# Optimization experiments

Hardware: AMD Instinct MI355X
Metric: run time of the kernel (lower is better)

The kernel has to match this reference:

```python
import jax, jax.numpy as jnp
import numpy as np

B, S, D, H, E = 2, 1024, 1024, 4096, 8


def _xavier(key, shape):
    # matches torch.nn.init.xavier_uniform_ on a 3D tensor: fan_in/out from last two dims
    fan_in, fan_out = shape[-2], shape[-1]
    limit = float(np.sqrt(6.0 / (fan_in + fan_out)))
    return jax.random.uniform(key, shape, jnp.float32, -limit, limit)


def setup_inputs() -> dict:
    key = jax.random.key(0)
    ks = jax.random.split(key, 4)
    x = jax.random.normal(ks[0], (B, S, D), jnp.float32)
    router_w = jax.random.normal(ks[1], (D, E), jnp.float32) * (1.0 / np.sqrt(D))
    router_b = jnp.zeros((E,), jnp.float32)
    fc1_weight = _xavier(ks[2], (E, D, H))
    fc1_bias = jnp.zeros((E, H), jnp.float32)
    fc2_weight = _xavier(ks[3], (E, H, D))
    fc2_bias = jnp.zeros((E, D), jnp.float32)
    return {
        "x": x,
        "router_w": router_w,
        "router_b": router_b,
        "fc1_weight": fc1_weight,
        "fc1_bias": fc1_bias,
        "fc2_weight": fc2_weight,
        "fc2_bias": fc2_bias,
    }


def reference(x, router_w, router_b, fc1_weight, fc1_bias, fc2_weight, fc2_bias):
    b, s, d = x.shape
    x_flat = x.reshape(-1, d)                                  # [T, D]
    logits = x_flat @ router_w + router_b                       # [T, E]
    probs = jax.nn.softmax(logits, axis=-1)                     # [T, E]
    # per-expert FC1 + exact GELU (torch nn.GELU default is erf-based)
    h = jnp.einsum('td,edh->teh', x_flat, fc1_weight) + fc1_bias  # [T, E, H]
    h = jax.nn.gelu(h, approximate=False)
    expert_out = jnp.einsum('teh,ehd->ted', h, fc2_weight) + fc2_bias  # [T, E, D]
    out_flat = jnp.einsum('te,ted->td', probs, expert_out)      # [T, D]
    y = out_flat.reshape(b, s, d)
    router_probs = probs.reshape(b, s, -1)
    return y, router_probs
```

## Files before the change

kernel.cpp:

```cpp
#include <hip/hip_runtime.h>
#include <math.h>


typedef float f32x4 __attribute__((ext_vector_type(4)));
typedef __bf16 bf16x8 __attribute__((ext_vector_type(8)));

#define GLL16(gp, lp)                                                          \
  __builtin_amdgcn_global_load_lds(                                            \
      (const __attribute__((address_space(1))) void*)(gp),                     \
      (__attribute__((address_space(3))) void*)(lp), 16, 0, 0)

__device__ __forceinline__ float gelu_f(float h) {
  return 0.5f * h * (1.f + erff(h * 0.70710678118654752f));
}

__global__ void router_kernel(const float* __restrict__ x,
                              const float* __restrict__ rw,
                              const float* __restrict__ rb,
                              float* __restrict__ P,
                              float* __restrict__ probs_out)
{
  int gid = blockIdx.x * blockDim.x + threadIdx.x;
  int t = gid >> 6;
  int l = gid & 63;
  const float* xr = x + (size_t)t * 1024;
  float a[8];
#pragma unroll
  for (int e = 0; e < 8; ++e) a[e] = 0.f;
  for (int d = l; d < 1024; d += 64) {
    float xv = xr[d];
    f32x4 w0 = *(const f32x4*)(rw + d * 8);
    f32x4 w1 = *(const f32x4*)(rw + d * 8 + 4);
#pragma unroll
    for (int e = 0; e < 4; ++e) a[e] += xv * w0[e];
#pragma unroll
    for (int e = 0; e < 4; ++e) a[4 + e] += xv * w1[e];
  }
#pragma unroll
  for (int off = 32; off > 0; off >>= 1) {
#pragma unroll
    for (int e = 0; e < 8; ++e) a[e] += __shfl_down(a[e], off);
  }
  if (l == 0) {
#pragma unroll
    for (int e = 0; e < 8; ++e) a[e] += rb[e];
    float m = a[0];
#pragma unroll
    for (int e = 1; e < 8; ++e) m = fmaxf(m, a[e]);
    float s = 0.f;
#pragma unroll
    for (int e = 0; e < 8; ++e) { a[e] = __expf(a[e] - m); s += a[e]; }
    float inv = 1.f / s;
#pragma unroll
    for (int e = 0; e < 8; ++e) {
      float p = a[e] * inv;
      if (P) P[t * 8 + e] = p;
      probs_out[t * 8 + e] = p;
    }
  }
}

__global__ void cvt_kernel(const float* __restrict__ src,
                           __bf16* __restrict__ dst)
{
  size_t i = ((size_t)blockIdx.x * 256 + threadIdx.x) * 8;
  f32x4 v0 = *(const f32x4*)(src + i);
  f32x4 v1 = *(const f32x4*)(src + i + 4);
  bf16x8 o;
#pragma unroll
  for (int j = 0; j < 4; ++j) o[j] = (__bf16)v0[j];
#pragma unroll
  for (int j = 0; j < 4; ++j) o[4 + j] = (__bf16)v1[j];
  *(bf16x8*)(dst + i) = o;
}

__global__ void transconv_kernel(const float* __restrict__ src,
                                 __bf16* __restrict__ dst,
                                 int R, int C, int cChunk,
                                 size_t dstLd, size_t zOff)
{
  size_t bs = (size_t)blockIdx.z * (size_t)R * (size_t)C;
  size_t dzo = (size_t)blockIdx.z * zOff;
  int r = blockIdx.x * 256 + threadIdx.x;
  int c0 = blockIdx.y * cChunk;
  const float* s = src + bs + (size_t)r * C;
  for (int c = c0; c < c0 + cChunk; c += 8) {
    f32x4 v0 = *(const f32x4*)(s + c);
    f32x4 v1 = *(const f32x4*)(s + c + 4);
    float vv[8] = {v0[0], v0[1], v0[2], v0[3], v1[0], v1[1], v1[2], v1[3]};
#pragma unroll
    for (int j = 0; j < 8; ++j)
      dst[(size_t)(c + j) * dstLd + dzo + r] = (__bf16)vv[j];
  }
}

__device__ __forceinline__ void mfma_loop256(
    const char* Ab, const char* Bb, size_t ldaB, size_t ldbB, int K,
    char* lds, f32x4 acc[8][4])
{
  const int tid = threadIdx.x;
  const int w = tid >> 6, l = tid & 63;
  const int wm = w >> 2, wn = w & 3;
  const int m16 = l & 15, q = l >> 4;
  const int posB = ((q ^ ((m16 >> 1) & 3)) << 4);
  const int aE = (wm * 128 + m16) * 64 + posB;
  const int bE = 16384 + (wn * 64 + m16) * 64 + posB;
  const int sc16 = (((l & 3) ^ ((l >> 3) & 3)) << 4);
  const size_t sAoff = (size_t)(w * 32 + (l >> 2)) * ldaB + sc16;
  const size_t sBoff = (size_t)(w * 32 + (l >> 2)) * ldbB + sc16;
  const int ldst = w * 32 * 64;
  const int NT = K >> 5;

#define STAGE256(u)                                                            \
  {                                                                            \
    char* dA = lds + (((u) & 3) * 32768) + ldst;                               \
    const char* gA = Ab + sAoff + ((size_t)(u) << 6);                          \
    GLL16(gA, dA);                                                             \
    GLL16(gA + 16 * ldaB, dA + 1024);                                          \
    char* dB = dA + 16384;                                                     \
    const char* gB = Bb + sBoff + ((size_t)(u) << 6);                          \
    GLL16(gB, dB);                                                             \
    GLL16(gB + 16 * ldbB, dB + 1024);                                          \
  }

#define KFRAGS(T)                                                              \
    const char* ring = lds + (((T) & 3) * 32768);                              \
    bf16x8 af[8], bv[4];                                                       \
    _Pragma("unroll") for (int mi = 0; mi < 8; ++mi)                           \
        af[mi] = *(const bf16x8*)(ring + aE + mi * 1024);                      \
    _Pragma("unroll") for (int nj = 0; nj < 4; ++nj)                           \
        bv[nj] = *(const bf16x8*)(ring + bE + nj * 1024);

#define KMFMA                                                                  \
    __builtin_amdgcn_sched_barrier(0);                                         \
    asm volatile("s_waitcnt lgkmcnt(0)" ::: "memory");                         \
    __builtin_amdgcn_sched_barrier(0);                                         \
    __builtin_amdgcn_s_setprio(1);                                             \
    _Pragma("unroll") for (int mi = 0; mi < 8; ++mi)                           \
      _Pragma("unroll") for (int nj = 0; nj < 4; ++nj)                         \
        acc[mi][nj] = __builtin_amdgcn_mfma_f32_16x16x32_bf16(                 \
            af[mi], bv[nj], acc[mi][nj], 0, 0, 0);                             \
    __builtin_amdgcn_s_setprio(0);                                             \
    __builtin_amdgcn_sched_barrier(0);

  STAGE256(0);
  STAGE256(1);
  STAGE256(2);
  asm volatile("s_waitcnt vmcnt(8)" ::: "memory");
  __builtin_amdgcn_s_barrier();

  int t = 0;
  for (; t < NT - 3; ++t) {
    KFRAGS(t);
    STAGE256(t + 3);
    KMFMA;
    asm volatile("s_waitcnt vmcnt(8)" ::: "memory");
    __builtin_amdgcn_s_barrier();
  }
  {
    KFRAGS(t);
    KMFMA;
    asm volatile("s_waitcnt vmcnt(0)" ::: "memory");
    __builtin_amdgcn_s_barrier();
  }
  ++t;
  {
    KFRAGS(t);
    KMFMA;
  }
  ++t;
  {
    KFRAGS(t);
    KMFMA;
  }
#undef STAGE256
#undef KFRAGS
#undef KMFMA
}

__device__ __forceinline__ int xcd_swz(int id, int nwg) {
  return ((nwg & 7) == 0) ? ((id & 7) * (nwg >> 3) + (id >> 3)) : id;
}

__global__ __launch_bounds__(512, 2) void gemm1_kernel(
    const __bf16* __restrict__ X, const __bf16* __restrict__ W1T,
    const float* __restrict__ b1, const float* __restrict__ P,
    __bf16* __restrict__ Hs, int hs_ld, int e_off, size_t b_zstride)
{
  __shared__ __align__(16) char lds[131072];
  const int nwg = gridDim.x * gridDim.y * gridDim.z;
  const int id = blockIdx.x + gridDim.x * (blockIdx.y + gridDim.y * blockIdx.z);
  const int wg = xcd_swz(id, nwg);
  const int bm = wg & 7;
  const int bn = (wg >> 3) % gridDim.y;
  const int z = wg / (gridDim.y << 3);
  const int e = z + e_off;

  f32x4 acc[8][4];
  const f32x4 z4 = {0.f, 0.f, 0.f, 0.f};
#pragma unroll
  for (int i = 0; i < 8; ++i)
#pragma unroll
    for (int j = 0; j < 4; ++j) acc[i][j] = z4;

  const char* A = (const char*)(X + (size_t)bm * 256 * 1024);
  const char* B = (const char*)(W1T + (size_t)z * b_zstride +
                                (size_t)bn * 256 * 1024);
  mfma_loop256(A, B, 2048, 2048, 1024, lds, acc);

  const int tid = threadIdx.x, w = tid >> 6, l = tid & 63;
  const int wm = w >> 2, wn = w & 3, q = l >> 4, m16 = l & 15;
  const int row0 = bm * 256 + wm * 128 + q * 4;
  const int colE = bn * 256 + wn * 64 + m16;
  const int zcol = (hs_ld == 4096) ? 0 : z * 4096;
  float b1v[4];
#pragma unroll
  for (int nj = 0; nj < 4; ++nj)
    b1v[nj] = b1[(size_t)e * 4096 + colE + nj * 16];
#pragma unroll
  for (int mi = 0; mi < 8; ++mi) {
    float pv[4];
#pragma unroll
    for (int r = 0; r < 4; ++r)
      pv[r] = P[(size_t)(row0 + mi * 16 + r) * 8 + e];
#pragma unroll
    for (int nj = 0; nj < 4; ++nj)
#pragma unroll
      for (int r = 0; r < 4; ++r) {
        float h = acc[mi][nj][r] + b1v[nj];
        float o = gelu_f(h) * pv[r];
        Hs[(size_t)(row0 + mi * 16 + r) * hs_ld + zcol + colE + nj * 16] =
            (__bf16)o;
      }
  }
}

__global__ __launch_bounds__(512, 2) void gemm2_kernel(
    const __bf16* __restrict__ Hs, const __bf16* __restrict__ W2T,
    float* __restrict__ accb, int lda, int ldb, int kz, int Kb)
{
  __shared__ __align__(16) char lds[131072];
  const int nwg = gridDim.x * gridDim.y * gridDim.z;
  const int id = blockIdx.x + gridDim.x * (blockIdx.y + gridDim.y * blockIdx.z);
  const int wg = xcd_swz(id, nwg);
  const int bm = wg & 7;
  const int bn = (wg >> 3) % gridDim.y;
  const int z = wg / (gridDim.y << 3);

  f32x4 acc[8][4];
  const f32x4 z4 = {0.f, 0.f, 0.f, 0.f};
#pragma unroll
  for (int i = 0; i < 8; ++i)
#pragma unroll
    for (int j = 0; j < 4; ++j) acc[i][j] = z4;

  const char* A = (const char*)(Hs + (size_t)bm * 256 * lda + (size_t)z * kz);
  const char* B = (const char*)(W2T + (size_t)bn * 256 * ldb + (size_t)z * kz);
  mfma_loop256(A, B, (size_t)lda * 2, (size_t)ldb * 2, Kb, lds, acc);

  const int tid = threadIdx.x, w = tid >> 6, l = tid & 63;
  const int wm = w >> 2, wn = w & 3, q = l >> 4, m16 = l & 15;
  const int row0 = bm * 256 + wm * 128 + q * 4;
  const int col0 = bn * 256 + wn * 64 + m16;
#pragma unroll
  for (int mi = 0; mi < 8; ++mi)
#pragma unroll
    for (int nj = 0; nj < 4; ++nj)
#pragma unroll
      for (int r = 0; r < 4; ++r)
        unsafeAtomicAdd(
            accb + (size_t)(row0 + mi * 16 + r) * 1024 + col0 + nj * 16,
            acc[mi][nj][r]);
}

__global__ void finalize_kernel(const float* __restrict__ accb,
                                const float* __restrict__ P,
                                const float* __restrict__ b2,
                                float* __restrict__ y)
{
  int idx = blockIdx.x * 256 + threadIdx.x;
  int t = idx >> 8;
  int d0 = (idx & 255) << 2;
  f32x4 a = *(const f32x4*)(accb + (size_t)t * 1024 + d0);
#pragma unroll
  for (int e = 0; e < 8; ++e) {
    float p = P[t * 8 + e];
    f32x4 b = *(const f32x4*)(b2 + (size_t)e * 1024 + d0);
#pragma unroll
    for (int c = 0; c < 4; ++c) a[c] += p * b[c];
  }
  *(f32x4*)(y + (size_t)t * 1024 + d0) = a;
}

__global__ __launch_bounds__(256) void fused_naive_kernel(
    const float* __restrict__ x, const float* __restrict__ w1,
    const float* __restrict__ b1, const float* __restrict__ w2,
    const float* __restrict__ b2, const float* __restrict__ probs,
    float* __restrict__ y)
{
  __shared__ float xs[8][1024];
  __shared__ float gs[8][64];
  __shared__ float ps[8];
  const int tid = threadIdx.x;
  const int t0 = blockIdx.x * 8;
  const size_t DH = (size_t)1024 * 4096;
  const int tt = tid >> 5;
  const int d0 = (tid & 31) * 32;
  float acc[32];
#pragma unroll
  for (int i = 0; i < 32; ++i) acc[i] = 0.f;
  {
    const f32x4* xsrc = (const f32x4*)(x + (size_t)t0 * 1024);
    f32x4* xdst = (f32x4*)&xs[0][0];
    for (int i = tid; i < 2048; i += 256) xdst[i] = xsrc[i];
  }
  const int wv = tid >> 6;
  const int hl = tid & 63;
  for (int e = 0; e < 8; ++e) {
    if (tid < 8) ps[tid] = probs[(size_t)(t0 + tid) * 8 + e];
    __syncthreads();
    for (int hc = 0; hc < 4096; hc += 64) {
      float a0 = 0.f, a1 = 0.f;
      const float* w1p = w1 + (size_t)e * DH + hc + hl;
      for (int d = 0; d < 1024; ++d) {
        float wvv = w1p[(size_t)d * 4096];
        a0 += xs[wv * 2 + 0][d] * wvv;
        a1 += xs[wv * 2 + 1][d] * wvv;
      }
      __syncthreads();
      gs[wv * 2 + 0][hl] =
          ps[wv * 2 + 0] * gelu_f(a0 + b1[(size_t)e * 4096 + hc + hl]);
      gs[wv * 2 + 1][hl] =
          ps[wv * 2 + 1] * gelu_f(a1 + b1[(size_t)e * 4096 + hc + hl]);
      __syncthreads();
      const float* w2p = w2 + (size_t)e * DH + (size_t)hc * 1024 + d0;
      for (int hh = 0; hh < 64; ++hh) {
        float g = gs[tt][hh];
#pragma unroll
        for (int jb = 0; jb < 8; ++jb) {
          f32x4 w4 = *(const f32x4*)(w2p + (size_t)hh * 1024 + jb * 4);
#pragma unroll
          for (int j2 = 0; j2 < 4; ++j2) acc[jb * 4 + j2] += g * w4[j2];
        }
      }
    }
#pragma unroll
    for (int j = 0; j < 32; ++j)
      acc[j] += ps[tt] * b2[(size_t)e * 1024 + d0 + j];
    __syncthreads();
  }
  float* yp = y + (size_t)(t0 + tt) * 1024 + d0;
#pragma unroll
  for (int jb = 0; jb < 8; ++jb) {
    f32x4 o = {acc[jb * 4], acc[jb * 4 + 1], acc[jb * 4 + 2], acc[jb * 4 + 3]};
    *(f32x4*)(yp + jb * 4) = o;
  }
}

extern "C" void kernel_launch(void* const* d_in, const int* in_sizes, int n_in,
                              void* d_out, int out_size, void* d_ws,
                              size_t ws_size, hipStream_t stream)
{
  const float* x  = (const float*)d_in[0];
  const float* rw = (const float*)d_in[1];
  const float* rb = (const float*)d_in[2];
  const float* w1 = (const float*)d_in[3];
  const float* b1 = (const float*)d_in[4];
  const float* w2 = (const float*)d_in[5];
  const float* b2 = (const float*)d_in[6];
  float* y = (float*)d_out;
  float* probs_out = y + (size_t)2048 * 1024;

  const size_t DH = (size_t)1024 * 4096;
  const size_t BASE = (64 << 10) + (size_t)2048 * 1024 * 4 +
                      (size_t)2048 * 1024 * 2;
  const size_t TA = BASE + 8 * DH * 2 + (size_t)2048 * 32768 * 2;
  const size_t TB = BASE + DH * 2 + (size_t)2048 * 4096 * 2;

  char* ws = (char*)d_ws;
  float* P = (float*)ws;
  float* accb = (float*)(ws + (64 << 10));
  __bf16* xb = (__bf16*)(ws + (64 << 10) + (size_t)2048 * 1024 * 4);
  char* ws2 = ws + BASE;

  if (ws_size >= TA) {
    router_kernel<<<512, 256, 0, stream>>>(x, rw, rb, P, probs_out);
    hipMemsetAsync(accb, 0, (size_t)2048 * 1024 * 4, stream);
    cvt_kernel<<<1024, 256, 0, stream>>>(x, xb);
    __bf16* WT = (__bf16*)ws2;
    __bf16* Hs = WT + 8 * DH;
    transconv_kernel<<<dim3(4, 64, 8), 256, 0, stream>>>(
        w1, WT, 1024, 4096, 64, 1024, DH);
    gemm1_kernel<<<dim3(8, 16, 8), 512, 0, stream>>>(xb, WT, b1, P, Hs,
                                                     32768, 0, DH);
    transconv_kernel<<<dim3(16, 16, 8), 256, 0, stream>>>(
        w2, WT, 4096, 1024, 64, 32768, 4096);
    gemm2_kernel<<<dim3(8, 4, 8), 512, 0, stream>>>(Hs, WT, accb, 32768,
                                                    32768, 4096, 4096);
    finalize_kernel<<<2048, 256, 0, stream>>>(accb, P, b2, y);
  } else if (ws_size >= TB) {
    router_kernel<<<512, 256, 0, stream>>>(x, rw, rb, P, probs_out);
    hipMemsetAsync(accb, 0, (size_t)2048 * 1024 * 4, stream);
    cvt_kernel<<<1024, 256, 0, stream>>>(x, xb);
    __bf16* WT = (__bf16*)ws2;
    __bf16* HsE = WT + DH;
    for (int e = 0; e < 8; ++e) {
      transconv_kernel<<<dim3(4, 64, 1), 256, 0, stream>>>(
          w1 + e * DH, WT, 1024, 4096, 64, 1024, 0);
      gemm1_kernel<<<dim3(8, 16, 1), 512, 0, stream>>>(xb, WT, b1, P, HsE,
                                                       4096, e, 0);
      transconv_kernel<<<dim3(16, 16, 1), 256, 0, stream>>>(
          w2 + e * DH, WT, 4096, 1024, 64, 4096, 0);
      gemm2_kernel<<<dim3(8, 4, 4), 512, 0, stream>>>(HsE, WT, accb, 4096,
                                                      4096, 1024, 1024);
    }
    finalize_kernel<<<2048, 256, 0, stream>>>(accb, P, b2, y);
  } else {
    router_kernel<<<512, 256, 0, stream>>>(x, rw, rb, (float*)nullptr,
                                           probs_out);
    fused_naive_kernel<<<256, 256, 0, stream>>>(x, w1, b1, w2, b2, probs_out,
                                                y);
  }
}
```

Before: 704.7 us.

## Approximate erf in GELU, widen transpose-convert stores, relax MFMA loop scheduling

Replaces the library erff in the GELU epilogue with an Abramowitz-Stegun polynomial that uses a hardware reciprocal and fast exp. The weight transpose-convert kernel now has each thread handle four rows, so it writes 4-element bf16 vectors instead of scalar bf16 stores, and its grids are shrunk to match. The GEMM inner loop loads B fragments first, drops the sched_barriers and the explicit lgkmcnt wait before the MFMAs, and merges that wait into the end-of-step barrier, leaving the compiler to interleave LDS reads with MFMAs. The erf approximation carries an error of roughly 1e-7 and could shift outputs slightly.

```diff
diff --git a/kernel.cpp b/kernel.cpp
--- a/kernel.cpp
+++ b/kernel.cpp
@@ -4,6 +4,7 @@
 
 typedef float f32x4 __attribute__((ext_vector_type(4)));
 typedef __bf16 bf16x8 __attribute__((ext_vector_type(8)));
+typedef __bf16 bf16x4 __attribute__((ext_vector_type(4)));
 
 #define GLL16(gp, lp)                                                          \
   __builtin_amdgcn_global_load_lds(                                            \
@@ -11,7 +12,17 @@
       (__attribute__((address_space(3))) void*)(lp), 16, 0, 0)
 
 __device__ __forceinline__ float gelu_f(float h) {
-  return 0.5f * h * (1.f + erff(h * 0.70710678118654752f));
+  float x = h * 0.70710678118654752f;
+  float ax = fabsf(x);
+  float t = __builtin_amdgcn_rcpf(fmaf(0.3275911f, ax, 1.0f));
+  float p = fmaf(1.061405429f, t, -1.453152027f);
+  p = fmaf(p, t, 1.421413741f);
+  p = fmaf(p, t, -0.284496736f);
+  p = fmaf(p, t, 0.254829592f);
+  float e = __expf(-x * x);
+  float erfv = fmaf(-p * t, e, 1.0f);
+  erfv = copysignf(erfv, x);
+  return 0.5f * h * (1.0f + erfv);
 }
 
 __global__ void router_kernel(const float* __restrict__ x,
@@ -81,16 +92,24 @@
 {
   size_t bs = (size_t)blockIdx.z * (size_t)R * (size_t)C;
   size_t dzo = (size_t)blockIdx.z * zOff;
-  int r = blockIdx.x * 256 + threadIdx.x;
+  int r0 = (blockIdx.x * 256 + threadIdx.x) * 4;
   int c0 = blockIdx.y * cChunk;
-  const float* s = src + bs + (size_t)r * C;
+  const float* s = src + bs + (size_t)r0 * C;
   for (int c = c0; c < c0 + cChunk; c += 8) {
-    f32x4 v0 = *(const f32x4*)(s + c);
-    f32x4 v1 = *(const f32x4*)(s + c + 4);
-    float vv[8] = {v0[0], v0[1], v0[2], v0[3], v1[0], v1[1], v1[2], v1[3]};
-#pragma unroll
-    for (int j = 0; j < 8; ++j)
-      dst[(size_t)(c + j) * dstLd + dzo + r] = (__bf16)vv[j];
+    float v[4][8];
+#pragma unroll
+    for (int rr = 0; rr < 4; ++rr) {
+      f32x4 a = *(const f32x4*)(s + (size_t)rr * C + c);
+      f32x4 b = *(const f32x4*)(s + (size_t)rr * C + c + 4);
+#pragma unroll
+      for (int j = 0; j < 4; ++j) { v[rr][j] = a[j]; v[rr][4 + j] = b[j]; }
+    }
+#pragma unroll
+    for (int j = 0; j < 8; ++j) {
+      bf16x4 o = {(__bf16)v[0][j], (__bf16)v[1][j], (__bf16)v[2][j],
+                  (__bf16)v[3][j]};
+      *(bf16x4*)(dst + (size_t)(c + j) * dstLd + dzo + r0) = o;
+    }
   }
 }
 
@@ -125,43 +144,40 @@
 
 #define KFRAGS(T)                                                              \
     const char* ring = lds + (((T) & 3) * 32768);                              \
-    bf16x8 af[8], bv[4];                                                       \
+    bf16x8 bv[4], af[8];                                                       \
+    _Pragma("unroll") for (int nj = 0; nj < 4; ++nj)                           \
+        bv[nj] = *(const bf16x8*)(ring + bE + nj * 1024);                      \
     _Pragma("unroll") for (int mi = 0; mi < 8; ++mi)                           \
-        af[mi] = *(const bf16x8*)(ring + aE + mi * 1024);                      \
-    _Pragma("unroll") for (int nj = 0; nj < 4; ++nj)                           \
-        bv[nj] = *(const bf16x8*)(ring + bE + nj * 1024);
+        af[mi] = *(const bf16x8*)(ring + aE + mi * 1024);
 
 #define KMFMA                                                                  \
-    __builtin_amdgcn_sched_barrier(0);                                         \
-    asm volatile("s_waitcnt lgkmcnt(0)" ::: "memory");                         \
-    __builtin_amdgcn_sched_barrier(0);                                         \
     __builtin_amdgcn_s_setprio(1);                                             \
     _Pragma("unroll") for (int mi = 0; mi < 8; ++mi)                           \
       _Pragma("unroll") for (int nj = 0; nj < 4; ++nj)                         \
         acc[mi][nj] = __builtin_amdgcn_mfma_f32_16x16x32_bf16(                 \
             af[mi], bv[nj], acc[mi][nj], 0, 0, 0);                             \
-    __builtin_amdgcn_s_setprio(0);                                             \
-    __builtin_amdgcn_sched_barrier(0);
+    __builtin_amdgcn_s_setprio(0);
+
+#define KSYNC(n)                                                               \
+    asm volatile("s_waitcnt vmcnt(" #n ") lgkmcnt(0)" ::: "memory");           \
+    __builtin_amdgcn_s_barrier();
 
   STAGE256(0);
   STAGE256(1);
   STAGE256(2);
-  asm volatile("s_waitcnt vmcnt(8)" ::: "memory");
-  __builtin_amdgcn_s_barrier();
+  KSYNC(8);
 
   int t = 0;
   for (; t < NT - 3; ++t) {
     KFRAGS(t);
     STAGE256(t + 3);
     KMFMA;
-    asm volatile("s_waitcnt vmcnt(8)" ::: "memory");
-    __builtin_amdgcn_s_barrier();
+    KSYNC(8);
   }
   {
     KFRAGS(t);
     KMFMA;
-    asm volatile("s_waitcnt vmcnt(0)" ::: "memory");
-    __builtin_amdgcn_s_barrier();
+    KSYNC(0);
   }
   ++t;
   {
@@ -176,6 +192,7 @@
 #undef STAGE256
 #undef KFRAGS
 #undef KMFMA
+#undef KSYNC
 }
 
 __device__ __forceinline__ int xcd_swz(int id, int nwg) {
@@ -389,11 +406,11 @@
     cvt_kernel<<<1024, 256, 0, stream>>>(x, xb);
     __bf16* WT = (__bf16*)ws2;
     __bf16* Hs = WT + 8 * DH;
-    transconv_kernel<<<dim3(4, 64, 8), 256, 0, stream>>>(
+    transconv_kernel<<<dim3(1, 64, 8), 256, 0, stream>>>(
         w1, WT, 1024, 4096, 64, 1024, DH);
     gemm1_kernel<<<dim3(8, 16, 8), 512, 0, stream>>>(xb, WT, b1, P, Hs,
                                                      32768, 0, DH);
-    transconv_kernel<<<dim3(16, 16, 8), 256, 0, stream>>>(
+    transconv_kernel<<<dim3(4, 16, 8), 256, 0, stream>>>(
         w2, WT, 4096, 1024, 64, 32768, 4096);
     gemm2_kernel<<<dim3(8, 4, 8), 512, 0, stream>>>(Hs, WT, accb, 32768,
                                                     32768, 4096, 4096);
@@ -405,11 +422,11 @@
     __bf16* WT = (__bf16*)ws2;
     __bf16* HsE = WT + DH;
     for (int e = 0; e < 8; ++e) {
-      transconv_kernel<<<dim3(4, 64, 1), 256, 0, stream>>>(
+      transconv_kernel<<<dim3(1, 64, 1), 256, 0, stream>>>(
           w1 + e * DH, WT, 1024, 4096, 64, 1024, 0);
       gemm1_kernel<<<dim3(8, 16, 1), 512, 0, stream>>>(xb, WT, b1, P, HsE,
                                                        4096, e, 0);
-      transconv_kernel<<<dim3(16, 16, 1), 256, 0, stream>>>(
+      transconv_kernel<<<dim3(4, 16, 1), 256, 0, stream>>>(
           w2 + e * DH, WT, 4096, 1024, 64, 4096, 0);
       gemm2_kernel<<<dim3(8, 4, 4), 512, 0, stream>>>(HsE, WT, accb, 4096,
                                                       4096, 1024, 1024);
```

Measured after the change: 728.8 us. +3.4%, slower.
